# Kernel tuning notes

Hardware: AMD Instinct MI355X
Metric: run time of the kernel (lower is better)

## Reference

```python
import jax, jax.numpy as jnp
import numpy as np

B, N, K = 8, 2048, 1024
MAXITER = 5


def hat(w):
    x, y, z = w[..., 0], w[..., 1], w[..., 2]
    O = jnp.zeros_like(x)
    return jnp.stack([
        jnp.stack([O, -z, y], -1),
        jnp.stack([z, O, -x], -1),
        jnp.stack([-y, x, O], -1)], -2)


def se3_exp(x):
    # x [..., 6] twist (w, v) -> [..., 4, 4] rigid transform
    w, v = x[..., :3], x[..., 3:]
    t = jnp.linalg.norm(w, axis=-1)
    small = t < 1e-6
    ts = jnp.where(small, 1.0, t)
    A = jnp.where(small, 1.0 - t * t / 6.0, jnp.sin(ts) / ts)
    Bc = jnp.where(small, 0.5 - t * t / 24.0, (1.0 - jnp.cos(ts)) / (ts * ts))
    Cc = jnp.where(small, 1.0 / 6.0 - t * t / 120.0, (ts - jnp.sin(ts)) / (ts ** 3))
    W = hat(w)
    W2 = W @ W
    I = jnp.eye(3, dtype=x.dtype)
    R = I + A[..., None, None] * W + Bc[..., None, None] * W2
    V = I + Bc[..., None, None] * W + Cc[..., None, None] * W2
    p = jnp.einsum('...ij,...j->...i', V, v)
    top = jnp.concatenate([R, p[..., None]], -1)              # [...,3,4]
    bot = jnp.zeros(top.shape[:-2] + (1, 4), x.dtype).at[..., 0, 3].set(1.0)
    return jnp.concatenate([top, bot], -2)


def transform(g, p):
    # g [...,4,4], p [...,n,3]
    R, t = g[..., :3, :3], g[..., :3, 3]
    return jnp.einsum('...ij,...nj->...ni', R, p) + t[..., None, :]


def encode(p, W1, b1, W2, b2, W3, b3):
    # shared-MLP PointNet 3->64->128->1024 + max pool over points
    h = jax.nn.relu(p @ W1 + b1)
    h = jax.nn.relu(h @ W2 + b2)
    h = h @ W3 + b3
    return h.max(axis=-2)


def setup_inputs() -> dict:
    key = jax.random.key(0)
    ks = jax.random.split(key, 8)
    inp = {
        'p_src': jax.random.normal(ks[0], (B, N, 3), jnp.float32),
        'p_tgt': jax.random.normal(ks[1], (B, N, 3), jnp.float32),
        'igt_twist': 0.1 * jax.random.normal(ks[2], (B, 6), jnp.float32),
        'dt': 0.01 * jnp.ones((1, 6), jnp.float32),
        'W1': jax.random.normal(ks[3], (3, 64), jnp.float32) / np.sqrt(3.0),
        'b1': jnp.zeros((64,), jnp.float32),
        'W2': jax.random.normal(ks[4], (64, 128), jnp.float32) / np.sqrt(64.0),
        'b2': jnp.zeros((128,), jnp.float32),
        'W3': jax.random.normal(ks[5], (128, 1024), jnp.float32) / np.sqrt(128.0),
        'b3': jnp.zeros((1024,), jnp.float32),
    }
    return inp


def reference(p_src, p_tgt, igt_twist, dt, W1, b1, W2, b2, W3, b3):
    bsz = p_src.shape[0]
    dtype = p_src.dtype
    eye4 = jnp.eye(4, dtype=dtype)

    # zero-mean normalization (p0 = target, p1 = source)
    p0_m = p_tgt.mean(axis=1)                     # [B,3]
    p1_m = p_src.mean(axis=1)
    q0 = p_tgt - p0_m[:, None, :]
    q1 = p_src - p1_m[:, None, :]
    a0 = jnp.tile(eye4, (bsz, 1, 1)).at[:, :3, 3].set(p0_m)
    a1 = jnp.tile(eye4, (bsz, 1, 1)).at[:, :3, 3].set(-p1_m)

    f0 = encode(q0, W1, b1, W2, b2, W3, b3)       # [B,K]

    # finite-difference Jacobian of feature wrt 6 twist params
    dtb = jnp.broadcast_to(dt, (bsz, 6))
    twists = -dtb[:, :, None] * jnp.eye(6, dtype=dtype)     # [B,6,6]
    transf = se3_exp(twists)                                 # [B,6,4,4]
    pj = transform(transf, q0[:, None, :, :])                # [B,6,N,3]
    fj = encode(pj, W1, b1, W2, b2, W3, b3)                  # [B,6,K]
    J = (f0[:, :, None] - jnp.swapaxes(fj, 1, 2)) / dtb[:, None, :]   # [B,K,6]

    Jt = jnp.swapaxes(J, 1, 2)                               # [B,6,K]
    H = Jt @ J                                               # [B,6,6]
    pinv = jnp.linalg.inv(H) @ Jt                            # [B,6,K]

    # IC Gauss-Newton iterations (fixed maxiter; xtol early-stop omitted for jit)
    g = jnp.tile(eye4, (bsz, 1, 1))
    r = None
    for _ in range(MAXITER):
        p = transform(g, q1)                                 # [B,N,3]
        f1 = encode(p, W1, b1, W2, b2, W3, b3)
        r = f1 - f0                                          # [B,K]
        dx = -jnp.einsum('bik,bk->bi', pinv, r)              # [B,6]
        g = se3_exp(dx) @ g

    est_g = a0 @ g @ a1                                      # undo zero-mean

    igt = se3_exp(igt_twist)
    loss_pp_wise = jnp.mean(jnp.abs(
        transform(est_g, p_src) - transform(jnp.linalg.inv(igt), p_src)))
    return r, loss_pp_wise
```

## Files before the change

### kernel.cpp

```cpp
#include <hip/hip_runtime.h>
#include <math.h>

#define BATCH 8
#define NPTS 2048
#define KF 1024

typedef _Float16 f16x8 __attribute__((ext_vector_type(8)));
typedef float f32x4 __attribute__((ext_vector_type(4)));

#define MFMA16(a,b,c) __builtin_amdgcn_mfma_f32_16x16x32_f16((a),(b),(c),0,0,0)

#define FSCALE 256.0f
#define INV16  (1.0f/65536.0f)

__device__ __forceinline__ void split_f16s(float x, _Float16& hi, _Float16& lo) {
  float xs = x * FSCALE;
  hi = (_Float16)xs;
  lo = (_Float16)(xs - (float)hi);
}

__device__ __forceinline__ void mat3mul(const float* A, const float* Bm, float* C) {
#pragma unroll
  for (int i = 0; i < 3; ++i)
#pragma unroll
    for (int j = 0; j < 3; ++j)
      C[i*3+j] = A[i*3+0]*Bm[0*3+j] + A[i*3+1]*Bm[1*3+j] + A[i*3+2]*Bm[2*3+j];
}

__device__ void se3_exp_dev(const float* x, float* R, float* p) {
  float wx = x[0], wy = x[1], wz = x[2];
  float vx = x[3], vy = x[4], vz = x[5];
  float t2 = wx*wx + wy*wy + wz*wz;
  float t = sqrtf(t2);
  float A, Bc, Cc;
  if (t < 1e-6f) {
    A  = 1.f - t2*(1.f/6.f);
    Bc = 0.5f - t2*(1.f/24.f);
    Cc = (1.f/6.f) - t2*(1.f/120.f);
  } else {
    float s = sinf(t), c = cosf(t);
    A  = s / t;
    Bc = (1.f - c) / t2;
    Cc = (t - s) / (t2 * t);
  }
  float W[9]  = {0.f, -wz, wy,  wz, 0.f, -wx,  -wy, wx, 0.f};
  float W2[9];
  mat3mul(W, W, W2);
#pragma unroll
  for (int i = 0; i < 9; ++i) {
    float I = (i == 0 || i == 4 || i == 8) ? 1.f : 0.f;
    R[i] = I + A*W[i] + Bc*W2[i];
  }
  float V[9];
#pragma unroll
  for (int i = 0; i < 9; ++i) {
    float I = (i == 0 || i == 4 || i == 8) ? 1.f : 0.f;
    V[i] = I + Bc*W[i] + Cc*W2[i];
  }
  p[0] = V[0]*vx + V[1]*vy + V[2]*vz;
  p[1] = V[3]*vx + V[4]*vy + V[5]*vz;
  p[2] = V[6]*vx + V[7]*vy + V[8]*vz;
}

__global__ void means_kernel(const float* __restrict__ tgt, const float* __restrict__ src,
                             float* __restrict__ mean_tgt, float* __restrict__ mean_src) {
  int which = blockIdx.x & 1, b = blockIdx.x >> 1;
  const float* p = (which ? src : tgt) + (size_t)b*NPTS*3;
  float* m = (which ? mean_src : mean_tgt) + b*3;
  int t = threadIdx.x;
  float s0 = 0.f, s1 = 0.f, s2 = 0.f;
  for (int i = t; i < NPTS; i += 256) {
    s0 += p[i*3+0]; s1 += p[i*3+1]; s2 += p[i*3+2];
  }
  __shared__ float red[256][3];
  red[t][0] = s0; red[t][1] = s1; red[t][2] = s2;
  __syncthreads();
  for (int s = 128; s > 0; s >>= 1) {
    if (t < s) { red[t][0] += red[t+s][0]; red[t][1] += red[t+s][1]; red[t][2] += red[t+s][2]; }
    __syncthreads();
  }
  if (t == 0) {
    m[0] = red[0][0] * (1.f/NPTS);
    m[1] = red[0][1] * (1.f/NPTS);
    m[2] = red[0][2] * (1.f/NPTS);
  }
}

__global__ void setup_kernel(const float* __restrict__ dt, const float* __restrict__ W1,
                             const float* __restrict__ b1, const float* __restrict__ igt_twist,
                             float* __restrict__ W1eff7, float* __restrict__ b1eff7,
                             float* __restrict__ W1effL, float* __restrict__ b1effL,
                             float* __restrict__ g_buf, float* __restrict__ igt_inv,
                             float* __restrict__ loss_out) {
  int t = threadIdx.x;
  for (int i = t; i < BATCH*192;  i += 256) W1effL[i] = W1[i % 192];
  for (int i = t; i < BATCH*64;   i += 256) b1effL[i] = b1[i & 63];
  if (t < 192) W1eff7[t] = W1[t];
  if (t < 64)  b1eff7[t] = b1[t];
  if (t < BATCH*16) {
    int i = t & 15;
    g_buf[t] = (i == 0 || i == 5 || i == 10 || i == 15) ? 1.f : 0.f;
  }
  if (t == 0) *loss_out = 0.f;
  if (t < 6) {
    float tw[6] = {0.f,0.f,0.f,0.f,0.f,0.f};
    tw[t] = -dt[t];
    float R[9], tr[3];
    se3_exp_dev(tw, R, tr);
    float* Wd = W1eff7 + (t+1)*192;
    for (int d = 0; d < 3; ++d)
      for (int c = 0; c < 64; ++c)
        Wd[d*64+c] = R[0*3+d]*W1[c] + R[1*3+d]*W1[64+c] + R[2*3+d]*W1[128+c];
    float* bd = b1eff7 + (t+1)*64;
    for (int c = 0; c < 64; ++c)
      bd[c] = b1[c] + tr[0]*W1[c] + tr[1]*W1[64+c] + tr[2]*W1[128+c];
  }
  if (t >= 32 && t < 32+BATCH) {
    int b = t - 32;
    float R[9], tr[3];
    se3_exp_dev(igt_twist + b*6, R, tr);
    float* inv = igt_inv + b*12;
    for (int r = 0; r < 3; ++r) {
      inv[r*4+0] = R[0*3+r];
      inv[r*4+1] = R[1*3+r];
      inv[r*4+2] = R[2*3+r];
      inv[r*4+3] = -(R[0*3+r]*tr[0] + R[1*3+r]*tr[1] + R[2*3+r]*tr[2]);
    }
  }
}

__global__ void pack_w3_kernel(const float* __restrict__ W3, _Float16* __restrict__ P) {
  int i = blockIdx.x*256 + threadIdx.x;
  int k = i >> 10, n = i & 1023;
  _Float16 hi, lo;
  split_f16s(W3[i], hi, lo);
  int nt = n >> 4, col = n & 15;
  int ks3 = k >> 5, rr = k & 31;
  int lane = (rr >> 3)*16 + col, jj = rr & 7;
  size_t base = (size_t)nt*4096;
  P[base + ((0*4 + ks3)*64 + lane)*8 + jj] = hi;
  P[base + ((1*4 + ks3)*64 + lane)*8 + jj] = lo;
}

__global__ void pack_w2_kernel(const float* __restrict__ W2,
                               _Float16* __restrict__ H, _Float16* __restrict__ L) {
  int i = blockIdx.x*256 + threadIdx.x;
  int k = i >> 7, n = i & 127;
  _Float16 hi, lo;
  split_f16s(W2[i], hi, lo);
  int nt2 = n >> 4, col = n & 15;
  int ks = k >> 5, rr = k & 31;
  int lane = (rr >> 3)*16 + col, jj = rr & 7;
  int dst = ((nt2*2 + ks)*64 + lane)*8 + jj;
  H[dst] = hi; L[dst] = lo;
}

__device__ __forceinline__ f32x4 zero4() {
  f32x4 z; z[0]=0.f; z[1]=0.f; z[2]=0.f; z[3]=0.f; return z;
}

__device__ __forceinline__ void l12_ptile(
    float px, float py, float pz,
    const float* __restrict__ w1, const float* __restrict__ bb1,
    const _Float16* __restrict__ W2h, const _Float16* __restrict__ W2l,
    const float* __restrict__ b2,
    _Float16* scr, int l, int lm, int q,
    f16x8 (&A3h)[4], f16x8 (&A3l)[4]) {
  f16x8 A2h[2], A2l[2];
#pragma unroll
  for (int ks = 0; ks < 2; ++ks) {
    const int c0 = ks*32 + q*8;
    float wa[8], wb[8], wc[8], bv[8];
    *(float4*)&wa[0] = *(const float4*)(w1 + c0);
    *(float4*)&wa[4] = *(const float4*)(w1 + c0 + 4);
    *(float4*)&wb[0] = *(const float4*)(w1 + 64 + c0);
    *(float4*)&wb[4] = *(const float4*)(w1 + 64 + c0 + 4);
    *(float4*)&wc[0] = *(const float4*)(w1 + 128 + c0);
    *(float4*)&wc[4] = *(const float4*)(w1 + 128 + c0 + 4);
    *(float4*)&bv[0] = *(const float4*)(bb1 + c0);
    *(float4*)&bv[4] = *(const float4*)(bb1 + c0 + 4);
#pragma unroll
    for (int jj = 0; jj < 8; ++jj) {
      float h = fmaf(px, wa[jj], fmaf(py, wb[jj], fmaf(pz, wc[jj], bv[jj])));
      h = fmaxf(h, 0.f);
      _Float16 hi, lo;
      split_f16s(h, hi, lo);
      A2h[ks][jj] = hi; A2l[ks][jj] = lo;
    }
  }
#pragma unroll
  for (int nt2 = 0; nt2 < 8; ++nt2) {
    f32x4 acc = zero4();
#pragma unroll
    for (int ks = 0; ks < 2; ++ks) {
      const int base = ((nt2*2 + ks)*64 + l)*8;
      const f16x8 Bh = *(const f16x8*)(W2h + base);
      const f16x8 Bl = *(const f16x8*)(W2l + base);
      acc = MFMA16(A2l[ks], Bh, acc);
      acc = MFMA16(A2h[ks], Bl, acc);
      acc = MFMA16(A2h[ks], Bh, acc);
    }
    const int c2 = nt2*16 + lm;
    const float b2v = b2[c2];
    const int ks3 = c2 >> 5;
    const int k31 = c2 & 31;
    const int qw = k31 >> 3, jw = k31 & 7;
#pragma unroll
    for (int r = 0; r < 4; ++r) {
      const int mrow = q*4 + r;
      float h = fmaxf(acc[r]*INV16 + b2v, 0.f);
      _Float16 hi, lo;
      split_f16s(h, hi, lo);
      const int idx = (ks3*64 + qw*16 + mrow)*8 + jw;
      scr[idx] = hi;
      scr[2048 + idx] = lo;
    }
  }
#pragma unroll
  for (int ks3 = 0; ks3 < 4; ++ks3) {
    const int base = (ks3*64 + l)*8;
    A3h[ks3] = *(const f16x8*)&scr[base];
    A3l[ks3] = *(const f16x8*)&scr[2048 + base];
  }
}

__global__ __launch_bounds__(256, 2) void encode_big(
    const float* __restrict__ pts, const float* __restrict__ mean,
    const float* __restrict__ W1e, const float* __restrict__ b1e,
    const _Float16* __restrict__ W2h, const _Float16* __restrict__ W2l,
    const _Float16* __restrict__ W3p, const float* __restrict__ b2,
    float* __restrict__ partial) {
  const int t = threadIdx.x;
  const int w = t >> 6, l = t & 63;
  const int lm = l & 15, q = l >> 4;
  const int pblk = blockIdx.x;
  const int j = blockIdx.y;
  const int b = blockIdx.z;

  __shared__ __align__(16) _Float16 smem[16384];

  const int ptbase = pblk*256 + w*64;
  float mx0 = mean[b*3+0], my0 = mean[b*3+1], mz0 = mean[b*3+2];
  const float* w1 = W1e + j*192;
  const float* bb1 = b1e + j*64;

  f16x8 A3h[4][4], A3l[4][4];
  _Float16* scr = smem + w*4096;
#pragma unroll
  for (int p = 0; p < 4; ++p) {
    const float* pp = pts + ((size_t)b*NPTS + ptbase + p*16 + lm)*3;
    l12_ptile(pp[0]-mx0, pp[1]-my0, pp[2]-mz0, w1, bb1, W2h, W2l, b2,
              scr, l, lm, q, A3h[p], A3l[p]);
  }
  __syncthreads();

  float* maxb = (float*)(smem + 8192);
  {
    f16x8 s0 = *(const f16x8*)(W3p + t*8);
    f16x8 s1 = *(const f16x8*)(W3p + 2048 + t*8);
    *(f16x8*)&smem[t*8] = s0;
    *(f16x8*)&smem[2048 + t*8] = s1;
  }
  __syncthreads();

  for (int k = 0; k < 64; ++k) {
    const int cur = (k & 1)*4096;
    const int nxt = cur ^ 4096;
    f16x8 s0, s1;
    const int have_next = (k + 1 < 64);
    if (have_next) {
      const _Float16* src = W3p + (size_t)(k+1)*4096;
      s0 = *(const f16x8*)(src + t*8);
      s1 = *(const f16x8*)(src + 2048 + t*8);
    }
    f16x8 B[2][4];
#pragma unroll
    for (int lev = 0; lev < 2; ++lev)
#pragma unroll
      for (int ks = 0; ks < 4; ++ks)
        B[lev][ks] = *(const f16x8*)&smem[cur + ((lev*4 + ks)*64 + l)*8];

    f32x4 a[4] = {zero4(), zero4(), zero4(), zero4()};
#pragma unroll
    for (int ks = 0; ks < 4; ++ks) {
#pragma unroll
      for (int p = 0; p < 4; ++p) a[p] = MFMA16(A3l[p][ks], B[0][ks], a[p]);
#pragma unroll
      for (int p = 0; p < 4; ++p) a[p] = MFMA16(A3h[p][ks], B[1][ks], a[p]);
#pragma unroll
      for (int p = 0; p < 4; ++p) a[p] = MFMA16(A3h[p][ks], B[0][ks], a[p]);
    }
    float mx = -INFINITY;
#pragma unroll
    for (int p = 0; p < 4; ++p)
#pragma unroll
      for (int r = 0; r < 4; ++r) mx = fmaxf(mx, a[p][r]);
    mx = fmaxf(mx, __shfl_xor(mx, 16, 64));
    mx = fmaxf(mx, __shfl_xor(mx, 32, 64));
    if (l < 16) maxb[w*1024 + k*16 + lm] = mx;

    if (have_next) {
      *(f16x8*)&smem[nxt + t*8] = s0;
      *(f16x8*)&smem[nxt + 2048 + t*8] = s1;
    }
    __syncthreads();
  }
  float* pout = partial + ((size_t)(j*BATCH + b)*8 + pblk)*KF;
  for (int f = t; f < KF; f += 256) {
    float m = fmaxf(fmaxf(maxb[f], maxb[1024+f]), fmaxf(maxb[2048+f], maxb[3072+f]));
    pout[f] = m*INV16;
  }
}

__global__ __launch_bounds__(512) void pinv_kernel(
    const float* __restrict__ partialB, const float* __restrict__ dt,
    float* __restrict__ pinvb, float* __restrict__ feats0) {
  const int b = blockIdx.x, t = threadIdx.x;
  float Jk2[2][6];
  float H[21];
#pragma unroll
  for (int i = 0; i < 21; ++i) H[i] = 0.f;
#pragma unroll
  for (int h = 0; h < 2; ++h) {
    const int kf = t + h*512;
    float fv[7];
#pragma unroll
    for (int j = 0; j < 7; ++j) {
      const float* ps = partialB + ((size_t)(j*BATCH + b)*8)*KF + kf;
      float m = ps[0];
#pragma unroll
      for (int s = 1; s < 8; ++s) m = fmaxf(m, ps[(size_t)s*KF]);
      fv[j] = m;
    }
    feats0[(size_t)b*KF + kf] = fv[0];
#pragma unroll
    for (int i = 0; i < 6; ++i) Jk2[h][i] = (fv[0] - fv[1+i]) / dt[i];
    int idx = 0;
#pragma unroll
    for (int i = 0; i < 6; ++i)
#pragma unroll
      for (int jj = i; jj < 6; ++jj) H[idx++] += Jk2[h][i]*Jk2[h][jj];
  }
#pragma unroll
  for (int i = 0; i < 21; ++i) {
    float v = H[i];
#pragma unroll
    for (int o = 1; o < 64; o <<= 1) v += __shfl_xor(v, o, 64);
    H[i] = v;
  }
  __shared__ float hred[8*21];
  __shared__ float s_hinv[36];
  const int wv = t >> 6, ln = t & 63;
  if (ln == 0)
#pragma unroll
    for (int i = 0; i < 21; ++i) hred[wv*21 + i] = H[i];
  __syncthreads();
  if (t == 0) {
    float Ht[21];
#pragma unroll
    for (int i = 0; i < 21; ++i) {
      float s = 0.f;
#pragma unroll
      for (int w2 = 0; w2 < 8; ++w2) s += hred[w2*21 + i];
      Ht[i] = s;
    }
    double L[6][6];
#pragma unroll
    for (int i = 0; i < 6; ++i)
#pragma unroll
      for (int j = 0; j <= i; ++j)
        L[i][j] = (double)Ht[j*6 - j*(j-1)/2 + (i - j)];
#pragma unroll
    for (int k = 0; k < 6; ++k) {
      double s = L[k][k];
#pragma unroll
      for (int m2 = 0; m2 < k; ++m2) s -= L[k][m2]*L[k][m2];
      double d = sqrt(s);
      double di = 1.0/d;
      L[k][k] = d;
#pragma unroll
      for (int i2 = k+1; i2 < 6; ++i2) {
        double s2 = L[i2][k];
#pragma unroll
        for (int m2 = 0; m2 < k; ++m2) s2 -= L[i2][m2]*L[k][m2];
        L[i2][k] = s2*di;
      }
    }
#pragma unroll
    for (int i2 = 0; i2 < 6; ++i2) {
      double dii = 1.0/L[i2][i2];
#pragma unroll
      for (int j2 = 0; j2 < i2; ++j2) {
        double s = 0.0;
#pragma unroll
        for (int k2 = j2; k2 < i2; ++k2) s += L[i2][k2]*L[k2][j2];
        L[i2][j2] = -dii*s;
      }
      L[i2][i2] = dii;
    }
#pragma unroll
    for (int i2 = 0; i2 < 6; ++i2)
#pragma unroll
      for (int j2 = 0; j2 <= i2; ++j2) {
        double s = 0.0;
#pragma unroll
        for (int k2 = i2; k2 < 6; ++k2) s += L[k2][i2]*L[k2][j2];
        s_hinv[i2*6+j2] = (float)s;
        s_hinv[j2*6+i2] = (float)s;
      }
  }
  __syncthreads();
#pragma unroll
  for (int h = 0; h < 2; ++h) {
    const int kf = t + h*512;
#pragma unroll
    for (int i = 0; i < 6; ++i) {
      float s = 0.f;
#pragma unroll
      for (int jj = 0; jj < 6; ++jj) s += s_hinv[i*6+jj] * Jk2[h][jj];
      pinvb[((size_t)b*6 + i)*KF + kf] = s;
    }
  }
}

__global__ __launch_bounds__(256, 3) void encode_loop(
    const float* __restrict__ pts, const float* __restrict__ mean,
    const float* __restrict__ W1e, const float* __restrict__ b1e,
    const _Float16* __restrict__ W2h, const _Float16* __restrict__ W2l,
    const _Float16* __restrict__ W3p, const float* __restrict__ b2,
    float* __restrict__ partial2) {
  const int t = threadIdx.x;
  const int w = t >> 6, l = t & 63;
  const int lm = l & 15, q = l >> 4;
  const int pblk = blockIdx.x;
  const int fg = blockIdx.y;
  const int b = blockIdx.z;
  const int nt0 = fg*16;

  __shared__ __align__(16) _Float16 smem[16384];

  const int pt = pblk*64 + w*16;
  float mx0 = mean[b*3+0], my0 = mean[b*3+1], mz0 = mean[b*3+2];
  const float* w1 = W1e + b*192;
  const float* bb1 = b1e + b*64;

  f16x8 A3h[4], A3l[4];
  {
    const float* pp = pts + ((size_t)b*NPTS + pt + lm)*3;
    l12_ptile(pp[0]-mx0, pp[1]-my0, pp[2]-mz0, w1, bb1, W2h, W2l, b2,
              smem + w*4096, l, lm, q, A3h, A3l);
  }
  __syncthreads();

  float* maxb = (float*)(smem + 8192);
  {
    const _Float16* src = W3p + (size_t)nt0*4096;
    f16x8 s0 = *(const f16x8*)(src + t*8);
    f16x8 s1 = *(const f16x8*)(src + 2048 + t*8);
    *(f16x8*)&smem[t*8] = s0;
    *(f16x8*)&smem[2048 + t*8] = s1;
  }
  __syncthreads();

  for (int k = 0; k < 16; ++k) {
    const int cur = (k & 1)*4096;
    const int nxt = cur ^ 4096;
    f16x8 s0, s1;
    const int have_next = (k + 1 < 16);
    if (have_next) {
      const _Float16* src = W3p + (size_t)(nt0 + k + 1)*4096;
      s0 = *(const f16x8*)(src + t*8);
      s1 = *(const f16x8*)(src + 2048 + t*8);
    }
    f16x8 B[2][4];
#pragma unroll
    for (int lev = 0; lev < 2; ++lev)
#pragma unroll
      for (int ks = 0; ks < 4; ++ks)
        B[lev][ks] = *(const f16x8*)&smem[cur + ((lev*4 + ks)*64 + l)*8];

    f32x4 a = zero4();
#pragma unroll
    for (int ks = 0; ks < 4; ++ks) {
      a = MFMA16(A3l[ks], B[0][ks], a);
      a = MFMA16(A3h[ks], B[1][ks], a);
      a = MFMA16(A3h[ks], B[0][ks], a);
    }
    float mx = fmaxf(fmaxf(a[0], a[1]), fmaxf(a[2], a[3]));
    mx = fmaxf(mx, __shfl_xor(mx, 16, 64));
    mx = fmaxf(mx, __shfl_xor(mx, 32, 64));
    if (l < 16) maxb[w*256 + k*16 + lm] = mx;

    if (have_next) {
      *(f16x8*)&smem[nxt + t*8] = s0;
      *(f16x8*)&smem[nxt + 2048 + t*8] = s1;
    }
    __syncthreads();
  }
  if (t < 256) {
    float m = fmaxf(fmaxf(maxb[t], maxb[256+t]), fmaxf(maxb[512+t], maxb[768+t]));
    partial2[((size_t)b*32 + pblk)*KF + fg*256 + t] = m*INV16;
  }
}

__global__ __launch_bounds__(1024) void update_kernel(
    const float* __restrict__ feats0, const float* __restrict__ partial2,
    const float* __restrict__ pinv, float* __restrict__ g_buf,
    const float* __restrict__ W1, const float* __restrict__ b1,
    float* __restrict__ W1effL, float* __restrict__ b1effL,
    float* __restrict__ r_out,
    const float* __restrict__ mean_tgt, const float* __restrict__ mean_src,
    float* __restrict__ est_g, int final_it) {
  const int b = blockIdx.x, t = threadIdx.x;
  const float* ps = partial2 + (size_t)b*32*KF + t;
  float m = ps[0];
#pragma unroll
  for (int s = 1; s < 32; ++s) m = fmaxf(m, ps[(size_t)s*KF]);
  float r = m - feats0[(size_t)b*KF + t];
  r_out[(size_t)b*KF + t] = r;
  float acc[6];
#pragma unroll
  for (int i = 0; i < 6; ++i) acc[i] = pinv[((size_t)b*6+i)*KF + t] * r;
#pragma unroll
  for (int i = 0; i < 6; ++i) {
    float v = acc[i];
#pragma unroll
    for (int o = 1; o < 64; o <<= 1) v += __shfl_xor(v, o, 64);
    acc[i] = v;
  }
  __shared__ float wred[16*6];
  const int wv = t >> 6, ln = t & 63;
  if (ln == 0)
#pragma unroll
    for (int i = 0; i < 6; ++i) wred[wv*6 + i] = acc[i];
  __syncthreads();
  __shared__ float s_g[16];
  if (t == 0) {
    float dx[6];
    for (int i = 0; i < 6; ++i) {
      float s = 0.f;
      for (int w2 = 0; w2 < 16; ++w2) s += wred[w2*6 + i];
      dx[i] = -s;
    }
    float R[9], p[3];
    se3_exp_dev(dx, R, p);
    float* g = g_buf + b*16;
    float gn[16];
    for (int r2 = 0; r2 < 3; ++r2)
      for (int c = 0; c < 4; ++c)
        gn[r2*4+c] = R[r2*3+0]*g[c] + R[r2*3+1]*g[4+c] + R[r2*3+2]*g[8+c] + p[r2]*g[12+c];
    gn[12] = 0.f; gn[13] = 0.f; gn[14] = 0.f; gn[15] = 1.f;
    for (int i = 0; i < 16; ++i) { g[i] = gn[i]; s_g[i] = gn[i]; }
    if (final_it) {
      const float* p0m = mean_tgt + b*3;
      const float* p1m = mean_src + b*3;
      float* e = est_g + b*12;
      for (int r2 = 0; r2 < 3; ++r2) {
        e[r2*4+0] = gn[r2*4+0];
        e[r2*4+1] = gn[r2*4+1];
        e[r2*4+2] = gn[r2*4+2];
        e[r2*4+3] = gn[r2*4+3]
                  - (gn[r2*4+0]*p1m[0] + gn[r2*4+1]*p1m[1] + gn[r2*4+2]*p1m[2])
                  + p0m[r2];
      }
    }
  }
  __syncthreads();
  if (!final_it) {
    if (t < 192) {
      int d = t >> 6, c = t & 63;
      W1effL[b*192 + t] = s_g[0*4+d]*W1[c] + s_g[1*4+d]*W1[64+c] + s_g[2*4+d]*W1[128+c];
    } else if (t < 256) {
      int i = t - 192;
      b1effL[b*64 + i] = b1[i] + s_g[3]*W1[i] + s_g[7]*W1[64+i] + s_g[11]*W1[128+i];
    }
  }
}

__global__ void loss_kernel(const float* __restrict__ p_src, const float* __restrict__ est_g,
                            const float* __restrict__ igt_inv, float* __restrict__ loss_out) {
  int b = blockIdx.y, tile = blockIdx.x, t = threadIdx.x;
  int n = tile*256 + t;
  const float* e = est_g + b*12;
  const float* v = igt_inv + b*12;
  const float* p = p_src + ((size_t)b*NPTS + n)*3;
  float px = p[0], py = p[1], pz = p[2];
  float s = 0.f;
#pragma unroll
  for (int r2 = 0; r2 < 3; ++r2) {
    float d1 = e[r2*4+0]*px + e[r2*4+1]*py + e[r2*4+2]*pz + e[r2*4+3];
    float d2 = v[r2*4+0]*px + v[r2*4+1]*py + v[r2*4+2]*pz + v[r2*4+3];
    s += fabsf(d1 - d2);
  }
  __shared__ float red[256];
  red[t] = s;
  __syncthreads();
  for (int st = 128; st > 0; st >>= 1) {
    if (t < st) red[t] += red[t+st];
    __syncthreads();
  }
  if (t == 0) atomicAdd(loss_out, red[0] * (1.f/((float)BATCH*NPTS*3)));
}

extern "C" void kernel_launch(void* const* d_in, const int* in_sizes, int n_in,
                              void* d_out, int out_size, void* d_ws, size_t ws_size,
                              hipStream_t stream) {
  const float* p_src     = (const float*)d_in[0];
  const float* p_tgt     = (const float*)d_in[1];
  const float* igt_twist = (const float*)d_in[2];
  const float* dt        = (const float*)d_in[3];
  const float* W1        = (const float*)d_in[4];
  const float* b1        = (const float*)d_in[5];
  const float* W2        = (const float*)d_in[6];
  const float* b2        = (const float*)d_in[7];
  const float* W3        = (const float*)d_in[8];
  float* out = (float*)d_out;

  float* ws = (float*)d_ws;
  float* mean_tgt = ws;  ws += 32;
  float* mean_src = ws;  ws += 32;
  float* W1eff7   = ws;  ws += 7*192;
  float* b1eff7   = ws;  ws += 7*64;
  float* feats0   = ws;  ws += BATCH*KF;
  float* W1effL   = ws;  ws += BATCH*192;
  float* b1effL   = ws;  ws += BATCH*64;
  float* g_buf    = ws;  ws += BATCH*16;
  float* pinvb    = ws;  ws += BATCH*6*KF;
  float* igt_inv  = ws;  ws += 96;
  float* est_g    = ws;  ws += 96;
  _Float16* W2h = (_Float16*)ws;  ws += 8192/2;
  _Float16* W2l = (_Float16*)ws;  ws += 8192/2;
  _Float16* W3p = (_Float16*)ws;  ws += 262144/2;
  float* partialB = ws;  ws += 56*8*KF;
  float* partial2 = ws;  ws += BATCH*32*KF;

  float* r_out    = out;
  float* loss_out = out + BATCH*KF;

  means_kernel<<<dim3(BATCH*2), 256, 0, stream>>>(p_tgt, p_src, mean_tgt, mean_src);
  setup_kernel<<<1, 256, 0, stream>>>(dt, W1, b1, igt_twist, W1eff7, b1eff7,
                                      W1effL, b1effL, g_buf, igt_inv, loss_out);
  pack_w2_kernel<<<dim3(8192/256), 256, 0, stream>>>(W2, W2h, W2l);
  pack_w3_kernel<<<dim3(131072/256), 256, 0, stream>>>(W3, W3p);

  encode_big<<<dim3(8, 7, BATCH), 256, 0, stream>>>(
      p_tgt, mean_tgt, W1eff7, b1eff7, W2h, W2l, W3p, b2, partialB);
  pinv_kernel<<<dim3(BATCH), 512, 0, stream>>>(partialB, dt, pinvb, feats0);

  for (int it = 0; it < 5; ++it) {
    encode_loop<<<dim3(32, 4, BATCH), 256, 0, stream>>>(
        p_src, mean_src, W1effL, b1effL, W2h, W2l, W3p, b2, partial2);
    update_kernel<<<dim3(BATCH), 1024, 0, stream>>>(
        feats0, partial2, pinvb, g_buf, W1, b1, W1effL, b1effL, r_out,
        mean_tgt, mean_src, est_g, (it == 4) ? 1 : 0);
  }
  loss_kernel<<<dim3(NPTS/256, BATCH), 256, 0, stream>>>(p_src, est_g, igt_inv, loss_out);
}
```

Baseline: 302.3 us.

## Merge setup kernels into one launch and fuse loss into final update

Four setup kernels (means, setup, W2 pack, W3 pack) become one prep kernel that branches on block index. The loss computation moves into the last update_kernel iteration, which keeps est_g in shared memory and reduces with wave shuffles. This removes the separate loss kernel and the est_g buffer. The 6x6 Cholesky inverse in pinv_kernel is also hand-unrolled into scalar doubles. The aim is to cut launch overhead and serial latency on small kernels, at the cost of the loss running on only 8 blocks.

```diff
diff --git a/kernel.cpp b/kernel.cpp
--- a/kernel.cpp
+++ b/kernel.cpp
@@ -62,97 +62,100 @@
   p[2] = V[6]*vx + V[7]*vy + V[8]*vz;
 }
 
-__global__ void means_kernel(const float* __restrict__ tgt, const float* __restrict__ src,
-                             float* __restrict__ mean_tgt, float* __restrict__ mean_src) {
-  int which = blockIdx.x & 1, b = blockIdx.x >> 1;
-  const float* p = (which ? src : tgt) + (size_t)b*NPTS*3;
-  float* m = (which ? mean_src : mean_tgt) + b*3;
-  int t = threadIdx.x;
-  float s0 = 0.f, s1 = 0.f, s2 = 0.f;
-  for (int i = t; i < NPTS; i += 256) {
-    s0 += p[i*3+0]; s1 += p[i*3+1]; s2 += p[i*3+2];
-  }
+__global__ void prep_kernel(
+    const float* __restrict__ p_src, const float* __restrict__ p_tgt,
+    const float* __restrict__ igt_twist, const float* __restrict__ dt,
+    const float* __restrict__ W1, const float* __restrict__ b1,
+    const float* __restrict__ W2, const float* __restrict__ W3,
+    float* __restrict__ mean_tgt, float* __restrict__ mean_src,
+    float* __restrict__ W1eff7, float* __restrict__ b1eff7,
+    float* __restrict__ W1effL, float* __restrict__ b1effL,
+    float* __restrict__ g_buf, float* __restrict__ igt_inv,
+    float* __restrict__ loss_out,
+    _Float16* __restrict__ W2h, _Float16* __restrict__ W2l,
+    _Float16* __restrict__ W3p) {
+  const int blk = blockIdx.x, t = threadIdx.x;
   __shared__ float red[256][3];
-  red[t][0] = s0; red[t][1] = s1; red[t][2] = s2;
-  __syncthreads();
-  for (int s = 128; s > 0; s >>= 1) {
-    if (t < s) { red[t][0] += red[t+s][0]; red[t][1] += red[t+s][1]; red[t][2] += red[t+s][2]; }
+  if (blk < 128) {
+#pragma unroll
+    for (int u = 0; u < 4; ++u) {
+      int i = blk*1024 + u*256 + t;
+      int k = i >> 10, n = i & 1023;
+      _Float16 hi, lo;
+      split_f16s(W3[i], hi, lo);
+      int nt = n >> 4, col = n & 15;
+      int ks3 = k >> 5, rr = k & 31;
+      int lane = (rr >> 3)*16 + col, jj = rr & 7;
+      size_t base = (size_t)nt*4096;
+      W3p[base + ((0*4 + ks3)*64 + lane)*8 + jj] = hi;
+      W3p[base + ((1*4 + ks3)*64 + lane)*8 + jj] = lo;
+    }
+  } else if (blk < 160) {
+    int i = (blk - 128)*256 + t;
+    int k = i >> 7, n = i & 127;
+    _Float16 hi, lo;
+    split_f16s(W2[i], hi, lo);
+    int nt2 = n >> 4, col = n & 15;
+    int ks = k >> 5, rr = k & 31;
+    int lane = (rr >> 3)*16 + col, jj = rr & 7;
+    int dst = ((nt2*2 + ks)*64 + lane)*8 + jj;
+    W2h[dst] = hi; W2l[dst] = lo;
+  } else if (blk < 176) {
+    int unit = blk - 160;
+    int which = unit & 1, b = unit >> 1;
+    const float* p = (which ? p_src : p_tgt) + (size_t)b*NPTS*3;
+    float* m = (which ? mean_src : mean_tgt) + b*3;
+    float s0 = 0.f, s1 = 0.f, s2 = 0.f;
+    for (int i = t; i < NPTS; i += 256) {
+      s0 += p[i*3+0]; s1 += p[i*3+1]; s2 += p[i*3+2];
+    }
+    red[t][0] = s0; red[t][1] = s1; red[t][2] = s2;
     __syncthreads();
-  }
-  if (t == 0) {
-    m[0] = red[0][0] * (1.f/NPTS);
-    m[1] = red[0][1] * (1.f/NPTS);
-    m[2] = red[0][2] * (1.f/NPTS);
-  }
-}
-
-__global__ void setup_kernel(const float* __restrict__ dt, const float* __restrict__ W1,
-                             const float* __restrict__ b1, const float* __restrict__ igt_twist,
-                             float* __restrict__ W1eff7, float* __restrict__ b1eff7,
-                             float* __restrict__ W1effL, float* __restrict__ b1effL,
-                             float* __restrict__ g_buf, float* __restrict__ igt_inv,
-                             float* __restrict__ loss_out) {
-  int t = threadIdx.x;
-  for (int i = t; i < BATCH*192;  i += 256) W1effL[i] = W1[i % 192];
-  for (int i = t; i < BATCH*64;   i += 256) b1effL[i] = b1[i & 63];
-  if (t < 192) W1eff7[t] = W1[t];
-  if (t < 64)  b1eff7[t] = b1[t];
-  if (t < BATCH*16) {
-    int i = t & 15;
-    g_buf[t] = (i == 0 || i == 5 || i == 10 || i == 15) ? 1.f : 0.f;
-  }
-  if (t == 0) *loss_out = 0.f;
-  if (t < 6) {
-    float tw[6] = {0.f,0.f,0.f,0.f,0.f,0.f};
-    tw[t] = -dt[t];
-    float R[9], tr[3];
-    se3_exp_dev(tw, R, tr);
-    float* Wd = W1eff7 + (t+1)*192;
-    for (int d = 0; d < 3; ++d)
+    for (int s = 128; s > 0; s >>= 1) {
+      if (t < s) { red[t][0] += red[t+s][0]; red[t][1] += red[t+s][1]; red[t][2] += red[t+s][2]; }
+      __syncthreads();
+    }
+    if (t == 0) {
+      m[0] = red[0][0] * (1.f/NPTS);
+      m[1] = red[0][1] * (1.f/NPTS);
+      m[2] = red[0][2] * (1.f/NPTS);
+    }
+  } else {
+    for (int i = t; i < BATCH*192;  i += 256) W1effL[i] = W1[i % 192];
+    for (int i = t; i < BATCH*64;   i += 256) b1effL[i] = b1[i & 63];
+    if (t < 192) W1eff7[t] = W1[t];
+    if (t < 64)  b1eff7[t] = b1[t];
+    if (t < BATCH*16) {
+      int i = t & 15;
+      g_buf[t] = (i == 0 || i == 5 || i == 10 || i == 15) ? 1.f : 0.f;
+    }
+    if (t == 0) *loss_out = 0.f;
+    if (t < 6) {
+      float tw[6] = {0.f,0.f,0.f,0.f,0.f,0.f};
+      tw[t] = -dt[t];
+      float R[9], tr[3];
+      se3_exp_dev(tw, R, tr);
+      float* Wd = W1eff7 + (t+1)*192;
+      for (int d = 0; d < 3; ++d)
+        for (int c = 0; c < 64; ++c)
+          Wd[d*64+c] = R[0*3+d]*W1[c] + R[1*3+d]*W1[64+c] + R[2*3+d]*W1[128+c];
+      float* bd = b1eff7 + (t+1)*64;
       for (int c = 0; c < 64; ++c)
-        Wd[d*64+c] = R[0*3+d]*W1[c] + R[1*3+d]*W1[64+c] + R[2*3+d]*W1[128+c];
-    float* bd = b1eff7 + (t+1)*64;
-    for (int c = 0; c < 64; ++c)
-      bd[c] = b1[c] + tr[0]*W1[c] + tr[1]*W1[64+c] + tr[2]*W1[128+c];
-  }
-  if (t >= 32 && t < 32+BATCH) {
-    int b = t - 32;
-    float R[9], tr[3];
-    se3_exp_dev(igt_twist + b*6, R, tr);
-    float* inv = igt_inv + b*12;
-    for (int r = 0; r < 3; ++r) {
-      inv[r*4+0] = R[0*3+r];
-      inv[r*4+1] = R[1*3+r];
-      inv[r*4+2] = R[2*3+r];
-      inv[r*4+3] = -(R[0*3+r]*tr[0] + R[1*3+r]*tr[1] + R[2*3+r]*tr[2]);
-    }
-  }
-}
-
-__global__ void pack_w3_kernel(const float* __restrict__ W3, _Float16* __restrict__ P) {
-  int i = blockIdx.x*256 + threadIdx.x;
-  int k = i >> 10, n = i & 1023;
-  _Float16 hi, lo;
-  split_f16s(W3[i], hi, lo);
-  int nt = n >> 4, col = n & 15;
-  int ks3 = k >> 5, rr = k & 31;
-  int lane = (rr >> 3)*16 + col, jj = rr & 7;
-  size_t base = (size_t)nt*4096;
-  P[base + ((0*4 + ks3)*64 + lane)*8 + jj] = hi;
-  P[base + ((1*4 + ks3)*64 + lane)*8 + jj] = lo;
-}
-
-__global__ void pack_w2_kernel(const float* __restrict__ W2,
-                               _Float16* __restrict__ H, _Float16* __restrict__ L) {
-  int i = blockIdx.x*256 + threadIdx.x;
-  int k = i >> 7, n = i & 127;
-  _Float16 hi, lo;
-  split_f16s(W2[i], hi, lo);
-  int nt2 = n >> 4, col = n & 15;
-  int ks = k >> 5, rr = k & 31;
-  int lane = (rr >> 3)*16 + col, jj = rr & 7;
-  int dst = ((nt2*2 + ks)*64 + lane)*8 + jj;
-  H[dst] = hi; L[dst] = lo;
+        bd[c] = b1[c] + tr[0]*W1[c] + tr[1]*W1[64+c] + tr[2]*W1[128+c];
+    }
+    if (t >= 32 && t < 32+BATCH) {
+      int b = t - 32;
+      float R[9], tr[3];
+      se3_exp_dev(igt_twist + b*6, R, tr);
+      float* inv = igt_inv + b*12;
+      for (int r = 0; r < 3; ++r) {
+        inv[r*4+0] = R[0*3+r];
+        inv[r*4+1] = R[1*3+r];
+        inv[r*4+2] = R[2*3+r];
+        inv[r*4+3] = -(R[0*3+r]*tr[0] + R[1*3+r]*tr[1] + R[2*3+r]*tr[2]);
+      }
+    }
+  }
 }
 
 __device__ __forceinline__ f32x4 zero4() {
@@ -364,50 +367,78 @@
       for (int w2 = 0; w2 < 8; ++w2) s += hred[w2*21 + i];
       Ht[i] = s;
     }
-    double L[6][6];
-#pragma unroll
-    for (int i = 0; i < 6; ++i)
-#pragma unroll
-      for (int j = 0; j <= i; ++j)
-        L[i][j] = (double)Ht[j*6 - j*(j-1)/2 + (i - j)];
-#pragma unroll
-    for (int k = 0; k < 6; ++k) {
-      double s = L[k][k];
-#pragma unroll
-      for (int m2 = 0; m2 < k; ++m2) s -= L[k][m2]*L[k][m2];
-      double d = sqrt(s);
-      double di = 1.0/d;
-      L[k][k] = d;
-#pragma unroll
-      for (int i2 = k+1; i2 < 6; ++i2) {
-        double s2 = L[i2][k];
-#pragma unroll
-        for (int m2 = 0; m2 < k; ++m2) s2 -= L[i2][m2]*L[k][m2];
-        L[i2][k] = s2*di;
-      }
-    }
-#pragma unroll
-    for (int i2 = 0; i2 < 6; ++i2) {
-      double dii = 1.0/L[i2][i2];
-#pragma unroll
-      for (int j2 = 0; j2 < i2; ++j2) {
-        double s = 0.0;
-#pragma unroll
-        for (int k2 = j2; k2 < i2; ++k2) s += L[i2][k2]*L[k2][j2];
-        L[i2][j2] = -dii*s;
-      }
-      L[i2][i2] = dii;
-    }
-#pragma unroll
-    for (int i2 = 0; i2 < 6; ++i2)
-#pragma unroll
-      for (int j2 = 0; j2 <= i2; ++j2) {
-        double s = 0.0;
-#pragma unroll
-        for (int k2 = i2; k2 < 6; ++k2) s += L[k2][i2]*L[k2][j2];
-        s_hinv[i2*6+j2] = (float)s;
-        s_hinv[j2*6+i2] = (float)s;
-      }
+    double h00=Ht[0], h01=Ht[1], h02=Ht[2], h03=Ht[3], h04=Ht[4], h05=Ht[5];
+    double h11=Ht[6], h12=Ht[7], h13=Ht[8], h14=Ht[9], h15=Ht[10];
+    double h22=Ht[11], h23=Ht[12], h24=Ht[13], h25=Ht[14];
+    double h33=Ht[15], h34=Ht[16], h35=Ht[17];
+    double h44=Ht[18], h45=Ht[19];
+    double h55=Ht[20];
+    double l00=sqrt(h00), i00=1.0/l00;
+    double l10=h01*i00, l20=h02*i00, l30=h03*i00, l40=h04*i00, l50=h05*i00;
+    double l11=sqrt(h11-l10*l10), i11=1.0/l11;
+    double l21=(h12-l20*l10)*i11;
+    double l31=(h13-l30*l10)*i11;
+    double l41=(h14-l40*l10)*i11;
+    double l51=(h15-l50*l10)*i11;
+    double l22=sqrt(h22-l20*l20-l21*l21), i22=1.0/l22;
+    double l32=(h23-l30*l20-l31*l21)*i22;
+    double l42=(h24-l40*l20-l41*l21)*i22;
+    double l52=(h25-l50*l20-l51*l21)*i22;
+    double l33=sqrt(h33-l30*l30-l31*l31-l32*l32), i33=1.0/l33;
+    double l43=(h34-l40*l30-l41*l31-l42*l32)*i33;
+    double l53=(h35-l50*l30-l51*l31-l52*l32)*i33;
+    double l44=sqrt(h44-l40*l40-l41*l41-l42*l42-l43*l43), i44=1.0/l44;
+    double l54=(h45-l50*l40-l51*l41-l52*l42-l53*l43)*i44;
+    double l55=sqrt(h55-l50*l50-l51*l51-l52*l52-l53*l53-l54*l54), i55=1.0/l55;
+    double m00=i00, m11=i11, m22=i22, m33=i33, m44=i44, m55=i55;
+    double m10=-i11*(l10*m00);
+    double m20=-i22*(l20*m00+l21*m10);
+    double m21=-i22*(l21*m11);
+    double m30=-i33*(l30*m00+l31*m10+l32*m20);
+    double m31=-i33*(l31*m11+l32*m21);
+    double m32=-i33*(l32*m22);
+    double m40=-i44*(l40*m00+l41*m10+l42*m20+l43*m30);
+    double m41=-i44*(l41*m11+l42*m21+l43*m31);
+    double m42=-i44*(l42*m22+l43*m32);
+    double m43=-i44*(l43*m33);
+    double m50=-i55*(l50*m00+l51*m10+l52*m20+l53*m30+l54*m40);
+    double m51=-i55*(l51*m11+l52*m21+l53*m31+l54*m41);
+    double m52=-i55*(l52*m22+l53*m32+l54*m42);
+    double m53=-i55*(l53*m33+l54*m43);
+    double m54=-i55*(l54*m44);
+    double v00 = m00*m00+m10*m10+m20*m20+m30*m30+m40*m40+m50*m50;
+    double v01 = m10*m11+m20*m21+m30*m31+m40*m41+m50*m51;
+    double v02 = m20*m22+m30*m32+m40*m42+m50*m52;
+    double v03 = m30*m33+m40*m43+m50*m53;
+    double v04 = m40*m44+m50*m54;
+    double v05 = m50*m55;
+    double v11 = m11*m11+m21*m21+m31*m31+m41*m41+m51*m51;
+    double v12 = m21*m22+m31*m32+m41*m42+m51*m52;
+    double v13 = m31*m33+m41*m43+m51*m53;
+    double v14 = m41*m44+m51*m54;
+    double v15 = m51*m55;
+    double v22 = m22*m22+m32*m32+m42*m42+m52*m52;
+    double v23 = m32*m33+m42*m43+m52*m53;
+    double v24 = m42*m44+m52*m54;
+    double v25 = m52*m55;
+    double v33 = m33*m33+m43*m43+m53*m53;
+    double v34 = m43*m44+m53*m54;
+    double v35 = m53*m55;
+    double v44 = m44*m44+m54*m54;
+    double v45 = m54*m55;
+    double v55 = m55*m55;
+    s_hinv[0]=(float)v00;  s_hinv[1]=(float)v01;  s_hinv[2]=(float)v02;
+    s_hinv[3]=(float)v03;  s_hinv[4]=(float)v04;  s_hinv[5]=(float)v05;
+    s_hinv[6]=(float)v01;  s_hinv[7]=(float)v11;  s_hinv[8]=(float)v12;
+    s_hinv[9]=(float)v13;  s_hinv[10]=(float)v14; s_hinv[11]=(float)v15;
+    s_hinv[12]=(float)v02; s_hinv[13]=(float)v12; s_hinv[14]=(float)v22;
+    s_hinv[15]=(float)v23; s_hinv[16]=(float)v24; s_hinv[17]=(float)v25;
+    s_hinv[18]=(float)v03; s_hinv[19]=(float)v13; s_hinv[20]=(float)v23;
+    s_hinv[21]=(float)v33; s_hinv[22]=(float)v34; s_hinv[23]=(float)v35;
+    s_hinv[24]=(float)v04; s_hinv[25]=(float)v14; s_hinv[26]=(float)v24;
+    s_hinv[27]=(float)v34; s_hinv[28]=(float)v44; s_hinv[29]=(float)v45;
+    s_hinv[30]=(float)v05; s_hinv[31]=(float)v15; s_hinv[32]=(float)v25;
+    s_hinv[33]=(float)v35; s_hinv[34]=(float)v45; s_hinv[35]=(float)v55;
   }
   __syncthreads();
 #pragma unroll
@@ -510,7 +541,8 @@
     float* __restrict__ W1effL, float* __restrict__ b1effL,
     float* __restrict__ r_out,
     const float* __restrict__ mean_tgt, const float* __restrict__ mean_src,
-    float* __restrict__ est_g, int final_it) {
+    const float* __restrict__ p_src, const float* __restrict__ igt_inv,
+    float* __restrict__ loss_out, int final_it) {
   const int b = blockIdx.x, t = threadIdx.x;
   const float* ps = partial2 + (size_t)b*32*KF + t;
   float m = ps[0];
@@ -535,6 +567,8 @@
     for (int i = 0; i < 6; ++i) wred[wv*6 + i] = acc[i];
   __syncthreads();
   __shared__ float s_g[16];
+  __shared__ float s_e[12];
+  __shared__ float s_v[12];
   if (t == 0) {
     float dx[6];
     for (int i = 0; i < 6; ++i) {
@@ -554,17 +588,17 @@
     if (final_it) {
       const float* p0m = mean_tgt + b*3;
       const float* p1m = mean_src + b*3;
-      float* e = est_g + b*12;
       for (int r2 = 0; r2 < 3; ++r2) {
-        e[r2*4+0] = gn[r2*4+0];
-        e[r2*4+1] = gn[r2*4+1];
-        e[r2*4+2] = gn[r2*4+2];
-        e[r2*4+3] = gn[r2*4+3]
-                  - (gn[r2*4+0]*p1m[0] + gn[r2*4+1]*p1m[1] + gn[r2*4+2]*p1m[2])
-                  + p0m[r2];
+        s_e[r2*4+0] = gn[r2*4+0];
+        s_e[r2*4+1] = gn[r2*4+1];
+        s_e[r2*4+2] = gn[r2*4+2];
+        s_e[r2*4+3] = gn[r2*4+3]
+                    - (gn[r2*4+0]*p1m[0] + gn[r2*4+1]*p1m[1] + gn[r2*4+2]*p1m[2])
+                    + p0m[r2];
       }
     }
   }
+  if (final_it && t >= 64 && t < 76) s_v[t-64] = igt_inv[b*12 + (t-64)];
   __syncthreads();
   if (!final_it) {
     if (t < 192) {
@@ -574,32 +608,29 @@
       int i = t - 192;
       b1effL[b*64 + i] = b1[i] + s_g[3]*W1[i] + s_g[7]*W1[64+i] + s_g[11]*W1[128+i];
     }
-  }
-}
-
-__global__ void loss_kernel(const float* __restrict__ p_src, const float* __restrict__ est_g,
-                            const float* __restrict__ igt_inv, float* __restrict__ loss_out) {
-  int b = blockIdx.y, tile = blockIdx.x, t = threadIdx.x;
-  int n = tile*256 + t;
-  const float* e = est_g + b*12;
-  const float* v = igt_inv + b*12;
-  const float* p = p_src + ((size_t)b*NPTS + n)*3;
-  float px = p[0], py = p[1], pz = p[2];
-  float s = 0.f;
-#pragma unroll
-  for (int r2 = 0; r2 < 3; ++r2) {
-    float d1 = e[r2*4+0]*px + e[r2*4+1]*py + e[r2*4+2]*pz + e[r2*4+3];
-    float d2 = v[r2*4+0]*px + v[r2*4+1]*py + v[r2*4+2]*pz + v[r2*4+3];
-    s += fabsf(d1 - d2);
-  }
-  __shared__ float red[256];
-  red[t] = s;
-  __syncthreads();
-  for (int st = 128; st > 0; st >>= 1) {
-    if (t < st) red[t] += red[t+st];
+  } else {
+    float ls = 0.f;
+    for (int n = t; n < NPTS; n += 1024) {
+      const float* p = p_src + ((size_t)b*NPTS + n)*3;
+      float px = p[0], py = p[1], pz = p[2];
+#pragma unroll
+      for (int r2 = 0; r2 < 3; ++r2) {
+        float d1 = s_e[r2*4+0]*px + s_e[r2*4+1]*py + s_e[r2*4+2]*pz + s_e[r2*4+3];
+        float d2 = s_v[r2*4+0]*px + s_v[r2*4+1]*py + s_v[r2*4+2]*pz + s_v[r2*4+3];
+        ls += fabsf(d1 - d2);
+      }
+    }
+#pragma unroll
+    for (int o = 1; o < 64; o <<= 1) ls += __shfl_xor(ls, o, 64);
+    __shared__ float lred[16];
+    if (ln == 0) lred[wv] = ls;
     __syncthreads();
-  }
-  if (t == 0) atomicAdd(loss_out, red[0] * (1.f/((float)BATCH*NPTS*3)));
+    if (t == 0) {
+      float s = 0.f;
+      for (int w2 = 0; w2 < 16; ++w2) s += lred[w2];
+      atomicAdd(loss_out, s * (1.f/((float)BATCH*NPTS*3)));
+    }
+  }
 }
 
 extern "C" void kernel_launch(void* const* d_in, const int* in_sizes, int n_in,
@@ -627,7 +658,6 @@
   float* g_buf    = ws;  ws += BATCH*16;
   float* pinvb    = ws;  ws += BATCH*6*KF;
   float* igt_inv  = ws;  ws += 96;
-  float* est_g    = ws;  ws += 96;
   _Float16* W2h = (_Float16*)ws;  ws += 8192/2;
   _Float16* W2l = (_Float16*)ws;  ws += 8192/2;
   _Float16* W3p = (_Float16*)ws;  ws += 262144/2;
@@ -637,11 +667,10 @@
   float* r_out    = out;
   float* loss_out = out + BATCH*KF;
 
-  means_kernel<<<dim3(BATCH*2), 256, 0, stream>>>(p_tgt, p_src, mean_tgt, mean_src);
-  setup_kernel<<<1, 256, 0, stream>>>(dt, W1, b1, igt_twist, W1eff7, b1eff7,
-                                      W1effL, b1effL, g_buf, igt_inv, loss_out);
-  pack_w2_kernel<<<dim3(8192/256), 256, 0, stream>>>(W2, W2h, W2l);
-  pack_w3_kernel<<<dim3(131072/256), 256, 0, stream>>>(W3, W3p);
+  prep_kernel<<<dim3(177), 256, 0, stream>>>(
+      p_src, p_tgt, igt_twist, dt, W1, b1, W2, W3,
+      mean_tgt, mean_src, W1eff7, b1eff7, W1effL, b1effL, g_buf, igt_inv,
+      loss_out, W2h, W2l, W3p);
 
   encode_big<<<dim3(8, 7, BATCH), 256, 0, stream>>>(
       p_tgt, mean_tgt, W1eff7, b1eff7, W2h, W2l, W3p, b2, partialB);
@@ -652,7 +681,6 @@
         p_src, mean_src, W1effL, b1effL, W2h, W2l, W3p, b2, partial2);
     update_kernel<<<dim3(BATCH), 1024, 0, stream>>>(
         feats0, partial2, pinvb, g_buf, W1, b1, W1effL, b1effL, r_out,
-        mean_tgt, mean_src, est_g, (it == 4) ? 1 : 0);
-  }
-  loss_kernel<<<dim3(NPTS/256, BATCH), 256, 0, stream>>>(p_src, est_g, igt_inv, loss_out);
-}
+        mean_tgt, mean_src, p_src, igt_inv, loss_out, (it == 4) ? 1 : 0);
+  }
+}
```

After: 290.8 us. -3.8%, faster.
